# Kernel optimization log

Measured on AMD Instinct MI355X. Metric: run time of the kernel, lower is better.

The kernel has to match this reference:

```python
import jax, jax.numpy as jnp
import numpy as np

B, E, P, BIT = 2048, 512, 4096, 64
H, HD, HID = 8, 64, 4096


def _l2norm(x, eps=1e-12):
    n = jnp.sqrt(jnp.sum(x * x, axis=1, keepdims=True))
    return x / jnp.maximum(n, eps)


def _mha(q, k, v, in_w, in_b, out_w, out_b):
    # torch.nn.MultiheadAttention, unbatched 2D input [L, E]
    qp = q @ in_w[:E].T + in_b[:E]
    kp = k @ in_w[E:2 * E].T + in_b[E:2 * E]
    vp = v @ in_w[2 * E:].T + in_b[2 * E:]
    L, S = q.shape[0], k.shape[0]
    qh = qp.reshape(L, H, HD).transpose(1, 0, 2)   # [H, L, HD]
    kh = kp.reshape(S, H, HD).transpose(1, 0, 2)
    vh = vp.reshape(S, H, HD).transpose(1, 0, 2)
    scores = jnp.einsum('hld,hsd->hls', qh, kh) / jnp.sqrt(jnp.float32(HD))
    attn = jax.nn.softmax(scores, axis=-1)
    out = jnp.einsum('hls,hsd->hld', attn, vh).transpose(1, 0, 2).reshape(L, E)
    return out @ out_w.T + out_b


def _mlp(x, W1, b1, W2, b2, Wc, bc):
    h = jax.nn.relu(x @ W1.T + b1)
    h = jax.nn.relu(h @ W2.T + b2)
    return _l2norm(h @ Wc.T + bc)


def setup_inputs():
    key = jax.random.key(0)
    ks = jax.random.split(key, 24)
    s = 0.02
    inp = {
        'image_feature': jax.random.normal(ks[0], (B, E), dtype=jnp.float32),
        'text_feature': jax.random.normal(ks[1], (B, E), dtype=jnp.float32),
        'prompts': jax.random.normal(ks[2], (P, E), dtype=jnp.float32),
        'img_in_w': jax.random.normal(ks[3], (3 * E, E), dtype=jnp.float32) * s,
        'img_in_b': jnp.zeros((3 * E,), jnp.float32),
        'img_out_w': jax.random.normal(ks[4], (E, E), dtype=jnp.float32) * s,
        'img_out_b': jnp.zeros((E,), jnp.float32),
        'txt_in_w': jax.random.normal(ks[5], (3 * E, E), dtype=jnp.float32) * s,
        'txt_in_b': jnp.zeros((3 * E,), jnp.float32),
        'txt_out_w': jax.random.normal(ks[6], (E, E), dtype=jnp.float32) * s,
        'txt_out_b': jnp.zeros((E,), jnp.float32),
        'img_W1': jax.random.normal(ks[7], (HID, 2 * E), dtype=jnp.float32) * s,
        'img_b1': jnp.zeros((HID,), jnp.float32),
        'img_W2': jax.random.normal(ks[8], (HID, HID), dtype=jnp.float32) * s,
        'img_b2': jnp.zeros((HID,), jnp.float32),
        'img_Wc': jax.random.normal(ks[9], (BIT, HID), dtype=jnp.float32) * s,
        'img_bc': jnp.zeros((BIT,), jnp.float32),
        'txt_W1': jax.random.normal(ks[10], (HID, 2 * E), dtype=jnp.float32) * s,
        'txt_b1': jnp.zeros((HID,), jnp.float32),
        'txt_W2': jax.random.normal(ks[11], (HID, HID), dtype=jnp.float32) * s,
        'txt_b2': jnp.zeros((HID,), jnp.float32),
        'txt_Wc': jax.random.normal(ks[12], (BIT, HID), dtype=jnp.float32) * s,
        'txt_bc': jnp.zeros((BIT,), jnp.float32),
        'iteration': 0,
    }
    return inp


def reference(image_feature, text_feature, prompts,
              img_in_w, img_in_b, img_out_w, img_out_b,
              txt_in_w, txt_in_b, txt_out_w, txt_out_b,
              img_W1, img_b1, img_W2, img_b2, img_Wc, img_bc,
              txt_W1, txt_b1, txt_W2, txt_b2, txt_Wc, txt_bc,
              iteration):
    # prompt_mode == 'share': cosine-sim matmul + argmax nearest-prompt + gather
    idx_i = jnp.argmax(image_feature @ prompts.T, axis=1)
    idx_t = jnp.argmax(text_feature @ prompts.T, axis=1)
    rm_i = prompts[idx_i]  # [B, E]
    rm_t = prompts[idx_t]
    enh_i = _mha(image_feature, rm_i, rm_i, img_in_w, img_in_b, img_out_w, img_out_b)
    enh_t = _mha(text_feature, rm_t, rm_t, txt_in_w, txt_in_b, txt_out_w, txt_out_b)
    fi = jnp.concatenate([image_feature, enh_i], axis=1)  # [B, 2E]
    ft = jnp.concatenate([text_feature, enh_t], axis=1)
    distill_i = _mlp(ft, img_W1, img_b1, img_W2, img_b2, img_Wc, img_bc)
    distill_t = _mlp(fi, txt_W1, txt_b1, txt_W2, txt_b2, txt_Wc, txt_bc)
    image_hash = _mlp(fi, img_W1, img_b1, img_W2, img_b2, img_Wc, img_bc)
    text_hash = _mlp(ft, txt_W1, txt_b1, txt_W2, txt_b2, txt_Wc, txt_bc)
    return (image_hash, text_hash, distill_i, distill_t)
```

## Files before the change

### kernel.cpp

```cpp
#include <hip/hip_runtime.h>
#include <cstdint>
#include <cstddef>

typedef _Float16 F16;
typedef _Float16 f16x8 __attribute__((ext_vector_type(8)));
typedef float f32x4 __attribute__((ext_vector_type(4)));

#define ASYNC_COPY16(gsrc, ldst)                                                        \
  __builtin_amdgcn_global_load_lds((const __attribute__((address_space(1))) void*)(gsrc), \
                                   (__attribute__((address_space(3))) void*)(ldst), 16, 0, 0)

constexpr int NCAST = 11;
struct CastJobs {
  const float* src[NCAST];
  F16* dst[NCAST];
  int nblk[NCAST];
};

__global__ __launch_bounds__(256) void cast_many(CastJobs j) {
  int rem = blockIdx.x;
  const float* src = j.src[0];
  F16* dst = j.dst[0];
  bool found = false;
#pragma unroll
  for (int s = 0; s < NCAST; ++s) {
    bool here = !found && (rem < j.nblk[s]);
    if (here) { src = j.src[s]; dst = j.dst[s]; found = true; }
    if (!found) rem -= j.nblk[s];
  }
  size_t i = ((size_t)rem * 256 + threadIdx.x) * 8;
  float4 a = *(const float4*)&src[i];
  float4 b = *(const float4*)&src[i + 4];
  f16x8 o;
  o[0] = (F16)a.x; o[1] = (F16)a.y; o[2] = (F16)a.z; o[3] = (F16)a.w;
  o[4] = (F16)b.x; o[5] = (F16)b.y; o[6] = (F16)b.z; o[7] = (F16)b.w;
  *(f16x8*)&dst[i] = o;
}

__global__ __launch_bounds__(256) void cast_one(const float* __restrict__ in,
                                                F16* __restrict__ out) {
  size_t i = ((size_t)blockIdx.x * 256 + threadIdx.x) * 8;
  float4 a = *(const float4*)&in[i];
  float4 b = *(const float4*)&in[i + 4];
  f16x8 o;
  o[0] = (F16)a.x; o[1] = (F16)a.y; o[2] = (F16)a.z; o[3] = (F16)a.w;
  o[4] = (F16)b.x; o[5] = (F16)b.y; o[6] = (F16)b.z; o[7] = (F16)b.w;
  *(f16x8*)&out[i] = o;
}

__global__ __launch_bounds__(256) void cast_half_cols(const float* __restrict__ src_i,
                                                      const float* __restrict__ src_t,
                                                      F16* __restrict__ fi, F16* __restrict__ ft) {
  int mod = blockIdx.z;
  const float* in = mod ? src_t : src_i;
  F16* out = mod ? ft : fi;
  int t = blockIdx.x * 256 + threadIdx.x;
  int i = t * 8;
  int row = i >> 9, c = i & 511;
  float4 a = *(const float4*)&in[(size_t)row * 512 + c];
  float4 b = *(const float4*)&in[(size_t)row * 512 + c + 4];
  f16x8 o;
  o[0] = (F16)a.x; o[1] = (F16)a.y; o[2] = (F16)a.z; o[3] = (F16)a.w;
  o[4] = (F16)b.x; o[5] = (F16)b.y; o[6] = (F16)b.z; o[7] = (F16)b.w;
  *(f16x8*)&out[(size_t)row * 1024 + c] = o;
}

__global__ __launch_bounds__(256) void argmax_part(const float* __restrict__ feat_i,
                                                   const float* __restrict__ feat_t,
                                                   const float* __restrict__ prompts,
                                                   float* __restrict__ pval, int* __restrict__ pidx) {
  const int mod = blockIdx.z;
  const float* feat = mod ? feat_t : feat_i;
  const int r0 = blockIdx.x * 64;
  const int p0 = blockIdx.y * 128;
  const int tid = threadIdx.x;
  const int tx = tid & 15, ty = tid >> 4;
  __shared__ __align__(16) float sA[64][36];
  __shared__ __align__(16) float sB[128][36];
  float acc[4][8] = {};
  for (int kt = 0; kt < 512; kt += 32) {
#pragma unroll
    for (int i = 0; i < 2; ++i) {
      int t = tid + 256 * i;
      int row = t >> 3, c = (t & 7) * 4;
      *(float4*)&sA[row][c] = *(const float4*)&feat[(size_t)(r0 + row) * 512 + kt + c];
    }
#pragma unroll
    for (int i = 0; i < 4; ++i) {
      int t = tid + 256 * i;
      int row = t >> 3, c = (t & 7) * 4;
      *(float4*)&sB[row][c] = *(const float4*)&prompts[(size_t)(p0 + row) * 512 + kt + c];
    }
    __syncthreads();
#pragma unroll
    for (int k = 0; k < 32; k += 4) {
      float4 a[4];
#pragma unroll
      for (int i = 0; i < 4; ++i) a[i] = *(const float4*)&sA[ty * 4 + i][k];
#pragma unroll
      for (int jj = 0; jj < 8; ++jj) {
        float4 b = *(const float4*)&sB[jj * 16 + tx][k];
#pragma unroll
        for (int i = 0; i < 4; ++i) {
          acc[i][jj] = fmaf(a[i].x, b.x, acc[i][jj]);
          acc[i][jj] = fmaf(a[i].y, b.y, acc[i][jj]);
          acc[i][jj] = fmaf(a[i].z, b.z, acc[i][jj]);
          acc[i][jj] = fmaf(a[i].w, b.w, acc[i][jj]);
        }
      }
    }
    __syncthreads();
  }
#pragma unroll
  for (int i = 0; i < 4; ++i) {
    float v = acc[i][0];
    int id = p0 + tx;
#pragma unroll
    for (int jj = 1; jj < 8; ++jj) {
      int idx = p0 + jj * 16 + tx;
      if (acc[i][jj] > v) { v = acc[i][jj]; id = idx; }
    }
#pragma unroll
    for (int off = 1; off < 16; off <<= 1) {
      float ov = __shfl_xor(v, off);
      int oi = __shfl_xor(id, off);
      if (ov > v || (ov == v && oi < id)) { v = ov; id = oi; }
    }
    if (tx == 0) {
      pval[((size_t)mod * 2048 + r0 + ty * 4 + i) * 32 + blockIdx.y] = v;
      pidx[((size_t)mod * 2048 + r0 + ty * 4 + i) * 32 + blockIdx.y] = id;
    }
  }
}

__global__ __launch_bounds__(256) void argmax_merge_gather(const float* __restrict__ pval,
                                                           const int* __restrict__ pidx,
                                                           const F16* __restrict__ prompts_h,
                                                           F16* __restrict__ rm_i,
                                                           F16* __restrict__ rm_t) {
  int tid = threadIdx.x;
  int w = tid >> 6, lane = tid & 63;
  int rowg = blockIdx.x * 4 + w;
  int mod = rowg >> 11, r = rowg & 2047;
  const float* pv = pval + ((size_t)mod * 2048 + r) * 32;
  const int* pi = pidx + ((size_t)mod * 2048 + r) * 32;
  float v = (lane < 32) ? pv[lane] : -3.4e38f;
  int id = (lane < 32) ? pi[lane] : 0x7fffffff;
#pragma unroll
  for (int off = 16; off; off >>= 1) {
    float ov = __shfl_down(v, off);
    int oi = __shfl_down(id, off);
    if (ov > v || (ov == v && oi < id)) { v = ov; id = oi; }
  }
  int bid = __shfl(id, 0);
  const F16* src = prompts_h + (size_t)bid * 512;
  F16* dst = (mod ? rm_t : rm_i) + (size_t)r * 512;
  *(f16x8*)(dst + lane * 8) = *(const f16x8*)(src + lane * 8);
}

struct Ptrs8 {
  const F16* A[8];
  const F16* B[8];
  const float* bias[8];
  void* D[8];
};

template <int BM, int BN, int WM, int WN, int ACT, int OUTF32, int L2N = 0, int KSPLIT = 1>
__global__ __launch_bounds__(256) void gemm_nt(Ptrs8 p, int K, int lda, int ldb, int ldd) {
  constexpr int SM = BM / WM, SN = BN / WN;
  constexpr int FM = SM / 16, FN = SN / 16;
  __shared__ __align__(16) F16 sA[BM * 32];
  __shared__ __align__(16) F16 sB[BN * 32];
  const int tid = threadIdx.x;
  const int lane = tid & 63, wid = tid >> 6;
  const int wr = wid / WN, wc = wid % WN;

  const int gx = gridDim.x, gy = gridDim.y;
  const int nwg = gx * gy * gridDim.z;
  int id = blockIdx.x + gx * (blockIdx.y + gy * blockIdx.z);
  id = (id & 7) * (nwg >> 3) + (id >> 3);
  const int bx = id % gx;
  const int tq = id / gx;
  const int by = tq % gy;
  const int bz = tq / gy;

  const F16* A = p.A[bz] + (size_t)bx * BM * lda;
  const F16* B = p.B[bz] + (KSPLIT > 1 ? (size_t)0 : (size_t)by * BN * ldb);
  const int k0 = (KSPLIT > 1) ? by * K : 0;

  f32x4 acc[FM][FN] = {};

  const int kfrag = (lane >> 4) * 8;
  const int kfx = kfrag ^ ((((lane & 15) >> 1) & 3) << 3);
  const int rA = wr * SM + (lane & 15);
  const int rB = wc * SN + (lane & 15);

  for (int kt = k0; kt < k0 + K; kt += 32) {
#pragma unroll
    for (int i = 0; i < (BM * 4) / 256; ++i) {
      int t = tid + 256 * i;
      int row = t >> 2;
      int c8 = (t & 3) ^ ((t >> 3) & 3);
      ASYNC_COPY16(A + (size_t)row * lda + kt + c8 * 8, sA + t * 8);
    }
#pragma unroll
    for (int i = 0; i < (BN * 4) / 256; ++i) {
      int t = tid + 256 * i;
      int row = t >> 2;
      int c8 = (t & 3) ^ ((t >> 3) & 3);
      ASYNC_COPY16(B + (size_t)row * ldb + kt + c8 * 8, sB + t * 8);
    }
    __syncthreads();
    f16x8 af[FM], bf[FN];
#pragma unroll
    for (int m = 0; m < FM; ++m) af[m] = *(const f16x8*)&sA[(rA + m * 16) * 32 + kfx];
#pragma unroll
    for (int n = 0; n < FN; ++n) bf[n] = *(const f16x8*)&sB[(rB + n * 16) * 32 + kfx];
#pragma unroll
    for (int m = 0; m < FM; ++m)
#pragma unroll
      for (int n = 0; n < FN; ++n)
        acc[m][n] = __builtin_amdgcn_mfma_f32_16x16x32_f16(af[m], bf[n], acc[m][n], 0, 0, 0);
    __syncthreads();
  }

  const float* bias = p.bias[bz];
  if constexpr (L2N) {
    __shared__ float sOut[64][68];
#pragma unroll
    for (int m = 0; m < FM; ++m)
#pragma unroll
      for (int n = 0; n < FN; ++n) {
        int c = wc * SN + n * 16 + (lane & 15);
        float bv = bias[c];
#pragma unroll
        for (int jj = 0; jj < 4; ++jj) {
          int r = wr * SM + m * 16 + (lane >> 4) * 4 + jj;
          sOut[r][c] = acc[m][n][jj] + bv;
        }
      }
    __syncthreads();
    int row = tid >> 2, q = tid & 3;
    float4 xv[4];
    float s = 0.f;
#pragma unroll
    for (int c4 = 0; c4 < 4; ++c4) {
      xv[c4] = *(const float4*)&sOut[row][q * 16 + c4 * 4];
      s += xv[c4].x * xv[c4].x + xv[c4].y * xv[c4].y + xv[c4].z * xv[c4].z + xv[c4].w * xv[c4].w;
    }
    s += __shfl_xor(s, 1);
    s += __shfl_xor(s, 2);
    float inv = 1.f / fmaxf(sqrtf(s), 1e-12f);
    float* D = (float*)p.D[bz] + (size_t)(bx * BM + row) * 64 + q * 16;
#pragma unroll
    for (int c4 = 0; c4 < 4; ++c4) {
      float4 o;
      o.x = xv[c4].x * inv; o.y = xv[c4].y * inv; o.z = xv[c4].z * inv; o.w = xv[c4].w * inv;
      *(float4*)&D[c4 * 4] = o;
    }
  } else {
    const int m0 = bx * BM + wr * SM;
    const int n0 = (KSPLIT > 1 ? 0 : by * BN) + wc * SN;
    float* Dks = nullptr;
    if (OUTF32)
      Dks = (float*)p.D[bz] + (KSPLIT > 1 ? (size_t)by * gx * BM * 64 : (size_t)0);
#pragma unroll
    for (int m = 0; m < FM; ++m) {
#pragma unroll
      for (int n = 0; n < FN; ++n) {
        int col = n0 + n * 16 + (lane & 15);
        float bv = (KSPLIT > 1 || !bias) ? 0.f : bias[col];
#pragma unroll
        for (int jj = 0; jj < 4; ++jj) {
          int row = m0 + m * 16 + (lane >> 4) * 4 + jj;
          float v = acc[m][n][jj] + bv;
          if (ACT) v = fmaxf(v, 0.f);
          if (OUTF32)
            Dks[(size_t)row * ldd + col] = v;
          else
            ((F16*)p.D[bz])[(size_t)row * ldd + col] = (F16)v;
        }
      }
    }
  }
}

__global__ __launch_bounds__(256) void reduce_l2norm(const float* __restrict__ part,
                                                     const float* __restrict__ bci,
                                                     const float* __restrict__ bct,
                                                     float* __restrict__ out) {
  int tid = threadIdx.x;
  int w = tid >> 6, lane = tid & 63;
  int rowg = blockIdx.x * 4 + w;
  int z = rowg >> 11, r = rowg & 2047;
  const float* pz = part + (((size_t)z * 4) * 2048 + r) * 64 + lane;
  float x = pz[0] + pz[(size_t)2048 * 64] + pz[(size_t)2 * 2048 * 64] + pz[(size_t)3 * 2048 * 64];
  x += ((z == 0 || z == 2) ? bci : bct)[lane];
  float s = x * x;
#pragma unroll
  for (int off = 32; off; off >>= 1) s += __shfl_xor(s, off);
  out[((size_t)z * 2048 + r) * 64 + lane] = x / fmaxf(sqrtf(s), 1e-12f);
}

__global__ __launch_bounds__(256) void softmax_rows(F16* __restrict__ s) {
  const size_t row = blockIdx.x;
  F16* p = s + row * 2048;
  const int tid = threadIdx.x;
  const int w = tid >> 6, lane = tid & 63;
  f16x8 v8 = *(const f16x8*)(p + tid * 8);
  float v[8];
#pragma unroll
  for (int j = 0; j < 8; ++j) v[j] = (float)v8[j];
  float m = -3.4e38f;
#pragma unroll
  for (int j = 0; j < 8; ++j) m = fmaxf(m, v[j]);
#pragma unroll
  for (int off = 32; off; off >>= 1) m = fmaxf(m, __shfl_xor(m, off));
  __shared__ float red[8];
  if (lane == 0) red[w] = m;
  __syncthreads();
  m = fmaxf(fmaxf(red[0], red[1]), fmaxf(red[2], red[3]));
  float sum = 0.f;
#pragma unroll
  for (int j = 0; j < 8; ++j) {
    v[j] = __expf((v[j] - m) * 0.125f);
    sum += v[j];
  }
#pragma unroll
  for (int off = 32; off; off >>= 1) sum += __shfl_xor(sum, off);
  if (lane == 0) red[4 + w] = sum;
  __syncthreads();
  sum = red[4] + red[5] + red[6] + red[7];
  float inv = 1.f / sum;
  f16x8 o;
#pragma unroll
  for (int j = 0; j < 8; ++j) o[j] = (F16)(v[j] * inv);
  *(f16x8*)(p + tid * 8) = o;
}

__global__ __launch_bounds__(256) void transpose_vp(const F16* __restrict__ qkv_i,
                                                    const F16* __restrict__ qkv_t,
                                                    F16* __restrict__ vpT_i, F16* __restrict__ vpT_t) {
  int mod = blockIdx.z;
  const F16* vp = (mod ? qkv_t : qkv_i) + 1024;
  F16* vpT = mod ? vpT_t : vpT_i;
  int s0 = blockIdx.x * 64, d0 = blockIdx.y * 64;
  __shared__ __align__(16) F16 tile[64][72];
  int tid = threadIdx.x;
#pragma unroll
  for (int i = 0; i < 2; ++i) {
    int ch = tid + 256 * i;
    int row = ch >> 3, c = (ch & 7) * 8;
    *(f16x8*)&tile[row][c] = *(const f16x8*)&vp[(size_t)(s0 + row) * 1536 + d0 + c];
  }
  __syncthreads();
#pragma unroll
  for (int i = 0; i < 2; ++i) {
    int ch = tid + 256 * i;
    int dr = ch >> 3, sc = (ch & 7) * 8;
    f16x8 o;
#pragma unroll
    for (int j = 0; j < 8; ++j) o[j] = tile[sc + j][dr];
    *(f16x8*)&vpT[(size_t)(d0 + dr) * 2048 + s0 + sc] = o;
  }
}

extern "C" void kernel_launch(void* const* d_in, const int* in_sizes, int n_in, void* d_out,
                              int out_size, void* d_ws, size_t ws_size, hipStream_t stream) {
  const float* img_f = (const float*)d_in[0];
  const float* txt_f = (const float*)d_in[1];
  const float* prompts = (const float*)d_in[2];
  const float* img_in_w = (const float*)d_in[3];
  const float* img_in_b = (const float*)d_in[4];
  const float* img_out_w = (const float*)d_in[5];
  const float* img_out_b = (const float*)d_in[6];
  const float* txt_in_w = (const float*)d_in[7];
  const float* txt_in_b = (const float*)d_in[8];
  const float* txt_out_w = (const float*)d_in[9];
  const float* txt_out_b = (const float*)d_in[10];
  const float* img_W1 = (const float*)d_in[11];
  const float* img_b1 = (const float*)d_in[12];
  const float* img_W2 = (const float*)d_in[13];
  const float* img_b2 = (const float*)d_in[14];
  const float* img_Wc = (const float*)d_in[15];
  const float* img_bc = (const float*)d_in[16];
  const float* txt_W1 = (const float*)d_in[17];
  const float* txt_b1 = (const float*)d_in[18];
  const float* txt_W2 = (const float*)d_in[19];
  const float* txt_b2 = (const float*)d_in[20];
  const float* txt_Wc = (const float*)d_in[21];
  const float* txt_bc = (const float*)d_in[22];
  float* out = (float*)d_out;

  char* ws = (char*)d_ws;
  size_t off = 0;
  auto alloc = [&](size_t bytes) -> void* {
    void* p = ws + off;
    off += (bytes + 255) & ~(size_t)255;
    return p;
  };
  F16* prompts_h = (F16*)alloc((size_t)4096 * 512 * 2);
  F16* in_w_i_h = (F16*)alloc((size_t)1536 * 512 * 2);
  F16* in_w_t_h = (F16*)alloc((size_t)1536 * 512 * 2);
  F16* out_w_i_h = (F16*)alloc((size_t)512 * 512 * 2);
  F16* out_w_t_h = (F16*)alloc((size_t)512 * 512 * 2);
  F16* W1_i = (F16*)alloc((size_t)4096 * 1024 * 2);
  F16* W1_t = (F16*)alloc((size_t)4096 * 1024 * 2);
  F16* Wc_i = (F16*)alloc((size_t)64 * 4096 * 2);
  F16* Wc_t = (F16*)alloc((size_t)64 * 4096 * 2);
  float* pval = (float*)alloc((size_t)2 * 2048 * 32 * 4);
  int* pidx = (int*)alloc((size_t)2 * 2048 * 32 * 4);
  F16* rm_i = (F16*)alloc((size_t)2048 * 512 * 2);
  F16* rm_t = (F16*)alloc((size_t)2048 * 512 * 2);
  F16* qkv_i = (F16*)alloc((size_t)2048 * 1536 * 2);
  F16* qkv_t = (F16*)alloc((size_t)2048 * 1536 * 2);
  F16* vpT_i = (F16*)alloc((size_t)512 * 2048 * 2);
  F16* vpT_t = (F16*)alloc((size_t)512 * 2048 * 2);
  F16* attn_i = (F16*)alloc((size_t)2048 * 512 * 2);
  F16* attn_t = (F16*)alloc((size_t)2048 * 512 * 2);
  F16* fi = (F16*)alloc((size_t)2048 * 1024 * 2);
  F16* ft = (F16*)alloc((size_t)2048 * 1024 * 2);
  float* wc_part = (float*)alloc((size_t)4 * 4 * 2048 * 64 * 4);
  F16* scores = (F16*)alloc((size_t)8 * 2048 * 2048 * 2);

  const size_t W2B = (size_t)4096 * 4096 * 2;
  const size_t H2B = (size_t)4 * 2048 * 4096 * 2;
  F16 *W2_i = nullptr, *W2_t = nullptr, *W2_shared = nullptr, *h2full = nullptr;
  int zb;
  if (off + 2 * W2B + H2B <= ws_size) {
    W2_i = (F16*)alloc(W2B); W2_t = (F16*)alloc(W2B); h2full = (F16*)alloc(H2B); zb = 4;
  } else if (off + 2 * W2B <= ws_size) {
    W2_i = (F16*)alloc(W2B); W2_t = (F16*)alloc(W2B); zb = 2;
  } else if (off + W2B <= ws_size) {
    W2_shared = (F16*)alloc(W2B); zb = 2;
  } else {
    return;
  }

  {
    CastJobs j;
    const int w2blk = W2_i ? 8192 : 0;
    const float* srcs[NCAST] = {img_W2, txt_W2, img_W1, txt_W1, prompts,
                                img_in_w, txt_in_w, img_out_w, txt_out_w, img_Wc, txt_Wc};
    F16* dsts[NCAST] = {W2_i ? W2_i : W2_shared, W2_t ? W2_t : W2_shared, W1_i, W1_t, prompts_h,
                        in_w_i_h, in_w_t_h, out_w_i_h, out_w_t_h, Wc_i, Wc_t};
    const int nb[NCAST] = {w2blk, w2blk, 2048, 2048, 1024, 384, 384, 128, 128, 128, 128};
    int total = 0;
    for (int s = 0; s < NCAST; ++s) { j.src[s] = srcs[s]; j.dst[s] = dsts[s]; j.nblk[s] = nb[s]; total += nb[s]; }
    cast_many<<<dim3(total), 256, 0, stream>>>(j);
  }
  cast_half_cols<<<dim3(512, 1, 2), 256, 0, stream>>>(img_f, txt_f, fi, ft);

  argmax_part<<<dim3(32, 32, 2), 256, 0, stream>>>(img_f, txt_f, prompts, pval, pidx);
  argmax_merge_gather<<<dim3(1024), 256, 0, stream>>>(pval, pidx, prompts_h, rm_i, rm_t);

  {
    Ptrs8 p{};
    p.A[0] = fi; p.B[0] = in_w_i_h; p.bias[0] = img_in_b; p.D[0] = qkv_i;
    p.A[1] = ft; p.B[1] = in_w_t_h; p.bias[1] = txt_in_b; p.D[1] = qkv_t;
    gemm_nt<128, 128, 2, 2, 0, 0><<<dim3(16, 4, 2), 256, 0, stream>>>(p, 512, 1024, 512, 1536);
  }
  {
    Ptrs8 p{};
    p.A[0] = rm_i; p.B[0] = in_w_i_h + (size_t)512 * 512; p.bias[0] = img_in_b + 512; p.D[0] = qkv_i + 512;
    p.A[1] = rm_t; p.B[1] = in_w_t_h + (size_t)512 * 512; p.bias[1] = txt_in_b + 512; p.D[1] = qkv_t + 512;
    gemm_nt<128, 128, 2, 2, 0, 0><<<dim3(16, 8, 2), 256, 0, stream>>>(p, 512, 512, 512, 1536);
  }
  transpose_vp<<<dim3(32, 8, 2), 256, 0, stream>>>(qkv_i, qkv_t, vpT_i, vpT_t);

  for (int mod = 0; mod < 2; ++mod) {
    F16* qkv = mod ? qkv_t : qkv_i;
    F16* vpT = mod ? vpT_t : vpT_i;
    F16* attn = mod ? attn_t : attn_i;
    {
      Ptrs8 p{};
      for (int h = 0; h < 8; ++h) {
        p.A[h] = qkv + h * 64;
        p.B[h] = qkv + 512 + h * 64;
        p.bias[h] = nullptr;
        p.D[h] = scores + (size_t)h * 2048 * 2048;
      }
      gemm_nt<128, 128, 2, 2, 0, 0><<<dim3(16, 16, 8), 256, 0, stream>>>(p, 64, 1536, 1536, 2048);
    }
    softmax_rows<<<dim3(16384), 256, 0, stream>>>(scores);
    {
      Ptrs8 p{};
      for (int h = 0; h < 8; ++h) {
        p.A[h] = scores + (size_t)h * 2048 * 2048;
        p.B[h] = vpT + (size_t)h * 64 * 2048;
        p.bias[h] = nullptr;
        p.D[h] = attn + h * 64;
      }
      gemm_nt<64, 64, 2, 2, 0, 0><<<dim3(32, 1, 8), 256, 0, stream>>>(p, 2048, 2048, 2048, 512);
    }
  }
  {
    Ptrs8 p{};
    p.A[0] = attn_i; p.B[0] = out_w_i_h; p.bias[0] = img_out_b; p.D[0] = fi + 512;
    p.A[1] = attn_t; p.B[1] = out_w_t_h; p.bias[1] = txt_out_b; p.D[1] = ft + 512;
    gemm_nt<128, 128, 2, 2, 0, 0><<<dim3(16, 4, 2), 256, 0, stream>>>(p, 512, 512, 512, 1024);
  }

  const int zlist[4] = {0, 2, 1, 3};
  const F16* mlpA[4] = {fi, ft, ft, fi};
  const float* mb1[4] = {img_b1, txt_b1, img_b1, txt_b1};
  const float* mb2[4] = {img_b2, txt_b2, img_b2, txt_b2};
  const F16* mW1[4] = {W1_i, W1_t, W1_i, W1_t};
  const F16* mWc[4] = {Wc_i, Wc_t, Wc_i, Wc_t};

  for (int b0 = 0; b0 < 4; b0 += zb) {
    F16* h1 = scores;
    F16* h2 = h2full ? h2full : scores + (size_t)zb * 2048 * 4096;
    {
      Ptrs8 p{};
      for (int q = 0; q < zb; ++q) {
        int z = zlist[b0 + q];
        p.A[q] = mlpA[z]; p.B[q] = mW1[z]; p.bias[q] = mb1[z];
        p.D[q] = h1 + (size_t)q * 2048 * 4096;
      }
      gemm_nt<128, 128, 2, 2, 1, 0><<<dim3(16, 32, zb), 256, 0, stream>>>(p, 1024, 1024, 1024, 4096);
    }
    {
      if (!W2_i) {
        const float* srcw2 = (zlist[b0] == 0 || zlist[b0] == 2) ? img_W2 : txt_W2;
        cast_one<<<dim3(8192), 256, 0, stream>>>(srcw2, W2_shared);
      }
      Ptrs8 p{};
      for (int q = 0; q < zb; ++q) {
        int z = zlist[b0 + q];
        const F16* wz = W2_i ? ((z == 0 || z == 2) ? W2_i : W2_t) : W2_shared;
        p.A[q] = h1 + (size_t)q * 2048 * 4096; p.B[q] = wz; p.bias[q] = mb2[z];
        p.D[q] = h2 + (size_t)q * 2048 * 4096;
      }
      gemm_nt<128, 128, 2, 2, 1, 0><<<dim3(16, 32, zb), 256, 0, stream>>>(p, 4096, 4096, 4096, 4096);
    }
    {
      Ptrs8 p{};
      for (int q = 0; q < zb; ++q) {
        int z = zlist[b0 + q];
        p.A[q] = h2 + (size_t)q * 2048 * 4096; p.B[q] = mWc[z]; p.bias[q] = nullptr;
        p.D[q] = wc_part + (size_t)z * 4 * 2048 * 64;
      }
      gemm_nt<64, 64, 2, 2, 0, 1, 0, 4><<<dim3(32, 4, zb), 256, 0, stream>>>(p, 1024, 4096, 4096, 64);
    }
  }
  reduce_l2norm<<<dim3(2048), 256, 0, stream>>>(wc_part, img_bc, txt_bc, out);
}
```

Measured before the change: 1.268 ms.

## Enlarge argmax GEMM tile to 128x128 with async LDS loads and XOR swizzle

```diff
diff --git a/kernel.cpp b/kernel.cpp
--- a/kernel.cpp
+++ b/kernel.cpp
@@ -65,60 +65,66 @@
   *(f16x8*)&out[(size_t)row * 1024 + c] = o;
 }
 
-__global__ __launch_bounds__(256) void argmax_part(const float* __restrict__ feat_i,
-                                                   const float* __restrict__ feat_t,
-                                                   const float* __restrict__ prompts,
-                                                   float* __restrict__ pval, int* __restrict__ pidx) {
+__global__ __launch_bounds__(256, 4) void argmax_part(const float* __restrict__ feat_i,
+                                                      const float* __restrict__ feat_t,
+                                                      const float* __restrict__ prompts,
+                                                      float* __restrict__ pval,
+                                                      int* __restrict__ pidx) {
   const int mod = blockIdx.z;
   const float* feat = mod ? feat_t : feat_i;
-  const int r0 = blockIdx.x * 64;
+  const int r0 = blockIdx.x * 128;
   const int p0 = blockIdx.y * 128;
   const int tid = threadIdx.x;
   const int tx = tid & 15, ty = tid >> 4;
-  __shared__ __align__(16) float sA[64][36];
-  __shared__ __align__(16) float sB[128][36];
-  float acc[4][8] = {};
+  __shared__ __align__(16) float sA[128 * 32];
+  __shared__ __align__(16) float sB[128 * 32];
+  float acc[8][8] = {};
+  const int swa = ty & 7;
+  const int swb = tx & 7;
   for (int kt = 0; kt < 512; kt += 32) {
 #pragma unroll
-    for (int i = 0; i < 2; ++i) {
-      int t = tid + 256 * i;
-      int row = t >> 3, c = (t & 7) * 4;
-      *(float4*)&sA[row][c] = *(const float4*)&feat[(size_t)(r0 + row) * 512 + kt + c];
-    }
-#pragma unroll
-    for (int i = 0; i < 4; ++i) {
-      int t = tid + 256 * i;
-      int row = t >> 3, c = (t & 7) * 4;
-      *(float4*)&sB[row][c] = *(const float4*)&prompts[(size_t)(p0 + row) * 512 + kt + c];
+    for (int it = 0; it < 4; ++it) {
+      int t = tid + 256 * it;
+      int row = t >> 3;
+      int c8 = (t & 7) ^ (row & 7);
+      ASYNC_COPY16(feat + (size_t)(r0 + row) * 512 + kt + c8 * 4, sA + t * 4);
+    }
+#pragma unroll
+    for (int it = 0; it < 4; ++it) {
+      int t = tid + 256 * it;
+      int row = t >> 3;
+      int c8 = (t & 7) ^ (row & 7);
+      ASYNC_COPY16(prompts + (size_t)(p0 + row) * 512 + kt + c8 * 4, sB + t * 4);
     }
     __syncthreads();
 #pragma unroll
-    for (int k = 0; k < 32; k += 4) {
-      float4 a[4];
-#pragma unroll
-      for (int i = 0; i < 4; ++i) a[i] = *(const float4*)&sA[ty * 4 + i][k];
-#pragma unroll
-      for (int jj = 0; jj < 8; ++jj) {
-        float4 b = *(const float4*)&sB[jj * 16 + tx][k];
-#pragma unroll
-        for (int i = 0; i < 4; ++i) {
-          acc[i][jj] = fmaf(a[i].x, b.x, acc[i][jj]);
-          acc[i][jj] = fmaf(a[i].y, b.y, acc[i][jj]);
-          acc[i][jj] = fmaf(a[i].z, b.z, acc[i][jj]);
-          acc[i][jj] = fmaf(a[i].w, b.w, acc[i][jj]);
+    for (int k4 = 0; k4 < 8; ++k4) {
+      float4 a[8];
+#pragma unroll
+      for (int i = 0; i < 8; ++i)
+        a[i] = *(const float4*)&sA[(ty + 16 * i) * 32 + (k4 ^ swa) * 4];
+#pragma unroll
+      for (int j = 0; j < 8; ++j) {
+        float4 b = *(const float4*)&sB[(tx + 16 * j) * 32 + (k4 ^ swb) * 4];
+#pragma unroll
+        for (int i = 0; i < 8; ++i) {
+          acc[i][j] = fmaf(a[i].x, b.x, acc[i][j]);
+          acc[i][j] = fmaf(a[i].y, b.y, acc[i][j]);
+          acc[i][j] = fmaf(a[i].z, b.z, acc[i][j]);
+          acc[i][j] = fmaf(a[i].w, b.w, acc[i][j]);
         }
       }
     }
     __syncthreads();
   }
 #pragma unroll
-  for (int i = 0; i < 4; ++i) {
+  for (int i = 0; i < 8; ++i) {
     float v = acc[i][0];
     int id = p0 + tx;
 #pragma unroll
-    for (int jj = 1; jj < 8; ++jj) {
-      int idx = p0 + jj * 16 + tx;
-      if (acc[i][jj] > v) { v = acc[i][jj]; id = idx; }
+    for (int j = 1; j < 8; ++j) {
+      int idx = p0 + j * 16 + tx;
+      if (acc[i][j] > v) { v = acc[i][j]; id = idx; }
     }
 #pragma unroll
     for (int off = 1; off < 16; off <<= 1) {
@@ -127,8 +133,8 @@
       if (ov > v || (ov == v && oi < id)) { v = ov; id = oi; }
     }
     if (tx == 0) {
-      pval[((size_t)mod * 2048 + r0 + ty * 4 + i) * 32 + blockIdx.y] = v;
-      pidx[((size_t)mod * 2048 + r0 + ty * 4 + i) * 32 + blockIdx.y] = id;
+      pval[((size_t)mod * 2048 + r0 + 16 * i + ty) * 32 + blockIdx.y] = v;
+      pidx[((size_t)mod * 2048 + r0 + 16 * i + ty) * 32 + blockIdx.y] = id;
     }
   }
 }
@@ -451,7 +457,7 @@
   }
   cast_half_cols<<<dim3(512, 1, 2), 256, 0, stream>>>(img_f, txt_f, fi, ft);
 
-  argmax_part<<<dim3(32, 32, 2), 256, 0, stream>>>(img_f, txt_f, prompts, pval, pidx);
+  argmax_part<<<dim3(16, 32, 2), 256, 0, stream>>>(img_f, txt_f, prompts, pval, pidx);
   argmax_merge_gather<<<dim3(1024), 256, 0, stream>>>(pval, pidx, prompts_h, rm_i, rm_t);
 
   {
```

Result: no change. 1.273 ms (+0.4%).
